# Performance work log

Measured on AMD Instinct MI355X. Metric: run time of the kernel, lower is better.

Reference implementation:

```python
import math
import jax, jax.numpy as jnp
import numpy as np

B, T, C = 4, 8192, 1024
EPS = 1e-5
LAYER_ID, N_LAYERS = 0, 24


def setup_inputs() -> dict:
    key = jax.random.key(0)
    ks = jax.random.split(key, 6)
    x = jax.random.normal(ks[0], (B, T, C), dtype=jnp.float32)
    # time_decay / time_first initialized exactly as in the torch __init__
    ratio_1_to_almost0 = 1.0 - LAYER_ID / N_LAYERS
    h = np.arange(C, dtype=np.float64)
    time_decay = (-5.0 + 8.0 * (h / (C - 1)) ** (0.7 + 1.3 * ratio_1_to_almost0)).astype(np.float32)
    zigzag = (((np.arange(C) + 1) % 3) - 1).astype(np.float32) * 0.5
    time_first = (math.log(0.3) + zigzag).astype(np.float32)
    # nn.Linear(dim, dim, bias=False) weights, stored as (out, in)
    std = 0.02
    Wk = jax.random.normal(ks[1], (C, C), dtype=jnp.float32) * std
    Wv = jax.random.normal(ks[2], (C, C), dtype=jnp.float32) * std
    Wr = jax.random.normal(ks[3], (C, C), dtype=jnp.float32) * std
    Wo = jax.random.normal(ks[4], (C, C), dtype=jnp.float32) * std
    ln_w = jnp.ones((C,), dtype=jnp.float32)
    ln_b = jnp.zeros((C,), dtype=jnp.float32)
    return {
        "x": x,
        "time_decay": jnp.asarray(time_decay),
        "time_first": jnp.asarray(time_first),
        "Wk": Wk, "Wv": Wv, "Wr": Wr, "Wo": Wo,
        "ln_w": ln_w, "ln_b": ln_b,
    }


def reference(x, time_decay, time_first, Wk, Wv, Wr, Wo, ln_w, ln_b):
    # LayerNorm (ln_x)
    mu = jnp.mean(x, axis=-1, keepdims=True)
    var = jnp.mean(jnp.square(x - mu), axis=-1, keepdims=True)
    xx = (x - mu) * jax.lax.rsqrt(var + EPS) * ln_w + ln_b

    # k, v, r projections (nn.Linear: y = x @ W^T)
    k = jnp.einsum('btc,dc->btd', xx, Wk)
    v = jnp.einsum('btc,dc->btd', xx, Wv)
    r = jnp.einsum('btc,dc->btd', xx, Wr)

    td = -jnp.exp(time_decay)   # (C,)
    tf = jnp.exp(time_first)    # (C,)

    # In the original loop, position j is weighted exp(td * j) regardless of t,
    # so wkv_history[t] = sum_{j < t} exp(td*j) * k[j] * v[j]  (exclusive cumsum).
    tpos = jnp.arange(T, dtype=jnp.float32)[:, None]        # (T,1)
    w = jnp.exp(td[None, :] * tpos)                         # (T,C)
    kv = k * v * w[None]                                    # (B,T,C)
    hist = jnp.cumsum(kv, axis=1) - kv                      # exclusive cumsum
    wkv = hist + k * tf

    out = jax.nn.sigmoid(r) * wkv
    return jnp.einsum('btc,dc->btd', out, Wo)
```

## Files before the change

### kernel.cpp

```cpp
#include <hip/hip_runtime.h>
#include <stdint.h>

#define B_ 4
#define T_ 8192
#define C_ 1024
#define BT_ (B_*T_)
#define NSEG 64
#define SLEN (T_/NSEG)
#define EPS_ 1e-5f
#define NT_ 16

typedef __attribute__((ext_vector_type(8))) short short8;
typedef __attribute__((ext_vector_type(4))) float float4v;
typedef __attribute__((ext_vector_type(4))) unsigned short ushort4v;
typedef unsigned short u16;

__device__ __forceinline__ u16 f2bf(float f){
  union { float f; uint32_t u; } v; v.f = f;
  uint32_t r = v.u + 0x7FFFu + ((v.u >> 16) & 1u);
  return (u16)(r >> 16);
}
__device__ __forceinline__ float bf2f(u16 h){
  union { uint32_t u; float f; } v; v.u = ((uint32_t)h) << 16;
  return v.f;
}
__device__ __forceinline__ void gload16(const void* g, void* l){
  __builtin_amdgcn_global_load_lds((__attribute__((address_space(1))) void*)(void*)g,
                                   (__attribute__((address_space(3))) void*)l,
                                   16, 0, 0);
}

__global__ void castw4_kernel(const float* __restrict__ s0, const float* __restrict__ s1,
                              const float* __restrict__ s2, const float* __restrict__ s3,
                              u16* __restrict__ dst){
  const float* src = (blockIdx.y==0)?s0:((blockIdx.y==1)?s1:((blockIdx.y==2)?s2:s3));
  u16* out = dst + (size_t)blockIdx.y*1048576;
  int i = blockIdx.x*blockDim.x + threadIdx.x;
  float4v v = ((const float4v*)src)[i];
  ushort4v o;
  o.x=f2bf(v.x); o.y=f2bf(v.y); o.z=f2bf(v.z); o.w=f2bf(v.w);
  ((ushort4v*)out)[i] = o;
}

__global__ __launch_bounds__(256) void ln_kernel(const float* __restrict__ x,
    const float* __restrict__ lw, const float* __restrict__ lb, u16* __restrict__ xxb)
{
  int row = blockIdx.x;
  int tid = threadIdx.x;
  float4v v = ((const float4v*)(x + (size_t)row*C_))[tid];
  float s1 = v.x+v.y+v.z+v.w;
  float s2 = v.x*v.x+v.y*v.y+v.z*v.z+v.w*v.w;
  #pragma unroll
  for (int off=32; off>0; off>>=1){
    s1 += __shfl_down(s1, off, 64);
    s2 += __shfl_down(s2, off, 64);
  }
  __shared__ float red1[4], red2[4];
  if ((tid&63)==0){ red1[tid>>6]=s1; red2[tid>>6]=s2; }
  __syncthreads();
  s1 = red1[0]+red1[1]+red1[2]+red1[3];
  s2 = red2[0]+red2[1]+red2[2]+red2[3];
  float mu = s1*(1.0f/C_);
  float rs = rsqrtf(s2*(1.0f/C_) - mu*mu + EPS_);
  float4v wv = ((const float4v*)lw)[tid];
  float4v bv = ((const float4v*)lb)[tid];
  ushort4v o;
  o.x = f2bf((v.x-mu)*rs*wv.x + bv.x);
  o.y = f2bf((v.y-mu)*rs*wv.y + bv.y);
  o.z = f2bf((v.z-mu)*rs*wv.z + bv.z);
  o.w = f2bf((v.w-mu)*rs*wv.w + bv.w);
  ((ushort4v*)(xxb + (size_t)row*C_))[tid] = o;
}

#define BAR() __builtin_amdgcn_s_barrier()

#define RD_A(DST, MH, BO) \
  _Pragma("unroll") for (int mt=0; mt<4; ++mt) \
    _Pragma("unroll") for (int ks=0; ks<2; ++ks) \
      DST[mt*2+ks] = *(const short8*)(lds + (BO) + ks*16384 + aoff0 + ((MH)*4+mt)*1024);

#define RD_B(DST, NH, BO) \
  _Pragma("unroll") for (int nt=0; nt<2; ++nt) \
    _Pragma("unroll") for (int ks=0; ks<2; ++ks) \
      DST[nt*2+ks] = *(const short8*)(lds + (BO) + ks*16384 + boff0 + ((NH)*2+nt)*1024);

#define MFMA_Q(AS, BS, MH, NH) do{ \
  __builtin_amdgcn_s_setprio(1); \
  _Pragma("unroll") for (int ks=0; ks<2; ++ks) \
    _Pragma("unroll") for (int mt=0; mt<4; ++mt) \
      _Pragma("unroll") for (int nt=0; nt<2; ++nt) \
        acc[(MH)*4+mt][(NH)*2+nt] = __builtin_amdgcn_mfma_f32_16x16x32_bf16( \
            AS[mt*2+ks], BS[nt*2+ks], acc[(MH)*4+mt][(NH)*2+nt], 0,0,0); \
  __builtin_amdgcn_s_setprio(0); \
}while(0)

template<bool F32OUT>
__global__ __launch_bounds__(512, 2) void gemm_dp(const u16* __restrict__ A,
    const u16* __restrict__ Bw, void* __restrict__ C0, void* __restrict__ C1,
    void* __restrict__ C2, int nbn)
{
  __shared__ __align__(1024) char lds[131072];

  const int tid  = threadIdx.x;
  const int lane = tid & 63;
  const int wid  = tid >> 6;
  const int wr   = wid >> 2;
  const int wc   = wid & 3;

  const int lin = blockIdx.x;
  const int x   = lin & 7;
  const int wl  = lin >> 3;
  const int bm  = x*16 + wl / nbn;
  const int bn  = wl % nbn;

  const int l15   = lane & 15;
  const int lswz  = ((lane>>4) ^ ((l15>>1)&3)) << 4;
  const int aoff0 = (wr*128 + l15)*64 + lswz;
  const int boff0 = 65536 + (wc*64 + l15)*64 + lswz;

  const int kk   = wid >> 2;
  const int rg0  = (wid & 3)*2;
  const int kkL  = kk*16384;
  const char* Asrc = ((const char*)A)  + ((size_t)bm*256 + (lane>>2))*2048
                     + (((lane&3) ^ ((lane>>3)&3)) << 4) + kk*64;
  const char* Bsrc = ((const char*)Bw) + ((size_t)bn*256 + (lane>>2))*2048
                     + (((lane&3) ^ ((lane>>3)&3)) << 4) + kk*64;

  float4v acc[8][4];
  float4v zero = {0.f,0.f,0.f,0.f};
  #pragma unroll
  for (int i=0;i<8;++i)
    #pragma unroll
    for (int j=0;j<4;++j) acc[i][j]=zero;

  auto stage = [&](int bo, int ktB){
    #pragma unroll
    for (int h=0; h<2; ++h)
      #pragma unroll
      for (int q=0; q<2; ++q){
        const int rowoff = h*128 + (rg0+q)*16;
        gload16(Asrc + (size_t)rowoff*2048 + ktB, lds + bo + kkL + rowoff*64);
        gload16(Bsrc + (size_t)rowoff*2048 + ktB, lds + 65536 + bo + kkL + rowoff*64);
      }
  };

  stage(0, 0);
  stage(32768, 128);
  asm volatile("s_waitcnt vmcnt(8)" ::: "memory");
  BAR();

  short8 A0r[8], A1r[8], B0r[4], B1r[4];

  #define TILE(KT, BO) do{ \
     \
    RD_A(A0r, 0, BO); RD_B(B0r, 0, BO); \
    BAR(); \
    MFMA_Q(A0r, B0r, 0, 0); \
    BAR(); \
     \
    RD_A(A1r, 1, BO); \
    BAR(); \
    MFMA_Q(A1r, B0r, 1, 0); \
    BAR(); \
     \
    RD_B(B1r, 1, BO); \
    BAR(); \
    MFMA_Q(A1r, B1r, 1, 1); \
    BAR(); \
     \
    if ((KT) < NT_-2) stage(BO, ((KT)+2)*128); \
    MFMA_Q(A0r, B1r, 0, 1); \
    if ((KT) < NT_-1){ \
      if ((KT) < NT_-2) { asm volatile("s_waitcnt vmcnt(8)" ::: "memory"); } \
      else              { asm volatile("s_waitcnt vmcnt(0)" ::: "memory"); } \
      BAR(); \
    } \
  }while(0)

  for (int kt2=0; kt2<NT_; kt2+=2){
    TILE(kt2,   0);
    TILE(kt2+1, 32768);
  }
  #undef TILE

  const int cl = l15, rq = lane >> 4;
  const size_t rbase = (size_t)bm*256 + wr*128;
  const int sel = bn >> 2;
  const int c0 = (bn&3)*256 + wc*64;
  void* cb = (sel==0) ? C0 : ((sel==1) ? C1 : C2);
  #pragma unroll
  for (int mi=0;mi<8;++mi)
    #pragma unroll
    for (int ni=0;ni<4;++ni)
      #pragma unroll
      for (int j=0;j<4;++j){
        size_t rr = rbase + mi*16 + rq*4 + j;
        int    cc = c0 + ni*16 + cl;
        if constexpr (F32OUT) ((float*)cb)[rr*1024 + cc] = acc[mi][ni][j];
        else                  ((u16*)cb)[rr*1024 + cc]   = f2bf(acc[mi][ni][j]);
      }
}

__global__ __launch_bounds__(256) void wkv_pass1(const u16* __restrict__ kb,
    const u16* __restrict__ vb, const float* __restrict__ tdecay,
    float* __restrict__ segsum)
{
  int c   = blockIdx.x*256 + threadIdx.x;
  int seg = blockIdx.y, b = blockIdx.z;
  float td = -expf(tdecay[c]);
  float d  = expf(td);
  int t0   = seg*SLEN;
  float w  = expf(td * (float)t0);
  size_t base = ((size_t)b*T_ + t0)*C_ + c;
  float s = 0.f;
  for (int i=0;i<SLEN;++i){
    float kk = bf2f(kb[base + (size_t)i*C_]);
    float vv = bf2f(vb[base + (size_t)i*C_]);
    s += kk*vv*w;
    w *= d;
  }
  segsum[((size_t)b*NSEG + seg)*C_ + c] = s;
}

__global__ void wkv_pass2(const float* __restrict__ segsum, float* __restrict__ segoff){
  int idx = blockIdx.x*256 + threadIdx.x;
  int b = idx / C_, c = idx % C_;
  float run = 0.f;
  for (int s=0;s<NSEG;++s){
    size_t o = ((size_t)b*NSEG + s)*C_ + c;
    segoff[o] = run;
    run += segsum[o];
  }
}

__global__ __launch_bounds__(256) void wkv_pass3(const u16* __restrict__ kb,
    const u16* __restrict__ vb, const u16* __restrict__ rb,
    const float* __restrict__ tdecay, const float* __restrict__ tfirst,
    const float* __restrict__ segoff, u16* __restrict__ outb)
{
  int c   = blockIdx.x*256 + threadIdx.x;
  int seg = blockIdx.y, b = blockIdx.z;
  float td = -expf(tdecay[c]);
  float d  = expf(td);
  float tf = expf(tfirst[c]);
  int t0   = seg*SLEN;
  float w  = expf(td * (float)t0);
  float hist = segoff[((size_t)b*NSEG + seg)*C_ + c];
  size_t base = ((size_t)b*T_ + t0)*C_ + c;
  for (int i=0;i<SLEN;++i){
    float kk = bf2f(kb[base + (size_t)i*C_]);
    float vv = bf2f(vb[base + (size_t)i*C_]);
    float rr = bf2f(rb[base + (size_t)i*C_]);
    float wkv = hist + kk*tf;
    float sg  = 1.f/(1.f + expf(-rr));
    outb[base + (size_t)i*C_] = f2bf(sg*wkv);
    hist += kk*vv*w;
    w *= d;
  }
}

extern "C" void kernel_launch(void* const* d_in, const int* in_sizes, int n_in,
                              void* d_out, int out_size, void* d_ws, size_t ws_size,
                              hipStream_t stream)
{
  (void)in_sizes; (void)n_in; (void)out_size; (void)ws_size;
  const float* x   = (const float*)d_in[0];
  const float* tdc = (const float*)d_in[1];
  const float* tfc = (const float*)d_in[2];
  const float* Wk  = (const float*)d_in[3];
  const float* Wv  = (const float*)d_in[4];
  const float* Wr  = (const float*)d_in[5];
  const float* Wo  = (const float*)d_in[6];
  const float* lw  = (const float*)d_in[7];
  const float* lb  = (const float*)d_in[8];
  float* out = (float*)d_out;

  char* ws = (char*)d_ws;
  u16* xxb = (u16*)(ws);
  u16* rb  = (u16*)(ws + 67108864);
  u16* Wkb = (u16*)(ws + 134217728);
  float* segsum = (float*)(ws + 142606336);
  float* segoff = (float*)(ws + 143654912);
  u16* kb = (u16*)d_out;
  u16* vb = kb + (size_t)BT_*C_;
  u16* outb = xxb;
  u16* Wob = Wkb + 3u*1048576u;

  castw4_kernel<<<dim3(1024,4),256,0,stream>>>(Wk, Wv, Wr, Wo, Wkb);

  ln_kernel<<<BT_,256,0,stream>>>(x, lw, lb, xxb);

  gemm_dp<false><<<1536,512,0,stream>>>(xxb, Wkb, kb, vb, rb, 12);

  dim3 sg(C_/256, NSEG, B_);
  wkv_pass1<<<sg,256,0,stream>>>(kb, vb, tdc, segsum);
  wkv_pass2<<<16,256,0,stream>>>(segsum, segoff);
  wkv_pass3<<<sg,256,0,stream>>>(kb, vb, rb, tdc, tfc, segoff, outb);

  gemm_dp<true><<<512,512,0,stream>>>(outb, Wob, out, out, out, 4);
}
```

Measured before the change: 501.8 us.

## Prefetch next K-tile LDS fragments during current tile MFMAs in GEMM

```diff
diff --git a/kernel.cpp b/kernel.cpp
--- a/kernel.cpp
+++ b/kernel.cpp
@@ -149,37 +149,37 @@
   asm volatile("s_waitcnt vmcnt(8)" ::: "memory");
   BAR();
 
-  short8 A0r[8], A1r[8], B0r[4], B1r[4];
-
-  #define TILE(KT, BO) do{ \
+  short8 Ax[8], Ay[8], Bp[4], Bq[4];
+  RD_A(Ax, 0, 0); RD_B(Bp, 0, 0);
+
+  #define TILE(KT, BO, BP, BQ) do{ \
      \
-    RD_A(A0r, 0, BO); RD_B(B0r, 0, BO); \
-    BAR(); \
-    MFMA_Q(A0r, B0r, 0, 0); \
+    RD_B(BQ, 1, BO); \
+    BAR(); \
+    MFMA_Q(Ax, BP, 0, 0); \
     BAR(); \
      \
-    RD_A(A1r, 1, BO); \
-    BAR(); \
-    MFMA_Q(A1r, B0r, 1, 0); \
+    RD_A(Ay, 1, BO); \
+    BAR(); \
+    MFMA_Q(Ax, BQ, 0, 1); \
+    if ((KT) < NT_-1){ asm volatile("s_waitcnt vmcnt(0)" ::: "memory"); } \
     BAR(); \
      \
-    RD_B(B1r, 1, BO); \
-    BAR(); \
-    MFMA_Q(A1r, B1r, 1, 1); \
+    if ((KT) < NT_-1){ RD_A(Ax, 0, (BO)^32768); } \
+    BAR(); \
+    MFMA_Q(Ay, BQ, 1, 1); \
     BAR(); \
      \
-    if ((KT) < NT_-2) stage(BO, ((KT)+2)*128); \
-    MFMA_Q(A0r, B1r, 0, 1); \
-    if ((KT) < NT_-1){ \
-      if ((KT) < NT_-2) { asm volatile("s_waitcnt vmcnt(8)" ::: "memory"); } \
-      else              { asm volatile("s_waitcnt vmcnt(0)" ::: "memory"); } \
-      BAR(); \
-    } \
+    if ((KT) < NT_-1){ RD_B(BQ, 0, (BO)^32768); } \
+    if ((KT) < NT_-2){ stage(BO, ((KT)+2)*128); } \
+    BAR(); \
+    MFMA_Q(Ay, BP, 1, 0); \
+    BAR(); \
   }while(0)
 
   for (int kt2=0; kt2<NT_; kt2+=2){
-    TILE(kt2,   0);
-    TILE(kt2+1, 32768);
+    TILE(kt2,   0,     Bp, Bq);
+    TILE(kt2+1, 32768, Bq, Bp);
   }
   #undef TILE
 
```

Measured after the change: 528.0 us. 5.2% more time.
